# Optimization experiments

Measured on AMD Instinct MI355X. Metric: run time of the kernel, lower is better.

The kernel has to match this reference:

```python
import jax, jax.numpy as jnp
import numpy as np

EPS = 1e-9
NEG_BIG = -1e9


def setup_inputs() -> dict:
    key = jax.random.key(0)
    kq, kk, kv, km = jax.random.split(key, 4)
    B, S, D = 2, 2048, 1024
    q = jax.random.normal(kq, (B, S, D), dtype=jnp.float32)
    k = jax.random.normal(kk, (B, S, D), dtype=jnp.float32)
    v = jax.random.normal(kv, (B, S, D), dtype=jnp.float32)
    mask = jax.random.randint(km, (S, S), 0, 2, dtype=jnp.int32)
    return {"q": q, "k": k, "v": v, "mask": mask, "num_heads": 16}


def _split_heads(x, num_heads):
    B, S, D = x.shape
    # [B, S, D] -> [B, H, S, dh]
    return x.reshape(B, S, num_heads, D // num_heads).transpose(0, 2, 1, 3)


def reference(q, k, v, mask, num_heads):
    B, S, D = q.shape
    dh = D // num_heads
    scale = dh ** (-0.5)
    qh = _split_heads(q, num_heads)  # [B,H,S,dh]
    kh = _split_heads(k, num_heads)
    vh = _split_heads(v, num_heads)
    # pairwise euclidean distance (cdist, p=2): sqrt(|q|^2 + |k|^2 - 2 q.k)
    q2 = jnp.sum(qh * qh, axis=-1)  # [B,H,S]
    k2 = jnp.sum(kh * kh, axis=-1)  # [B,H,S]
    qk = jnp.einsum("bhqd,bhkd->bhqk", qh, kh)
    d2 = q2[..., :, None] + k2[..., None, :] - 2.0 * qk
    dist = jnp.sqrt(jnp.maximum(d2, 0.0)) * scale  # [B,H,S,S]
    attn = 1.0 / (dist + EPS)
    attn = attn + mask.astype(jnp.float32)[None, None] * NEG_BIG
    attn = jax.nn.softmax(attn, axis=-1)
    # dropout is identity in eval / p=0.0
    x = jnp.einsum("bhqk,bhkd->bhqd", attn, vh)
    # [B,H,S,dh] -> [B,S,D]
    return x.transpose(0, 2, 1, 3).reshape(B, S, D)
```

## Files before the change

kernel.cpp:

```cpp
#include <hip/hip_runtime.h>
#include <hip/hip_bf16.h>
#include <math.h>

namespace {

constexpr int S  = 2048;
constexpr int D  = 1024;
constexpr int H  = 16;
constexpr int DH = 64;
constexpr int QB = 32;
constexpr int KT = 64;
constexpr float NEG_BIG = -1e9f;

typedef __attribute__((ext_vector_type(8))) short short8;
typedef __attribute__((ext_vector_type(4))) float f32x4;

union Frag {
  unsigned u[4];
  short8 v;
};

__device__ __forceinline__ unsigned bf16bits(float f) {
  __hip_bfloat16 h = __float2bfloat16(f);
  unsigned short us;
  __builtin_memcpy(&us, &h, 2);
  return (unsigned)us;
}
__device__ __forceinline__ unsigned pk2(float e, float o) {
  return bf16bits(e) | (bf16bits(o) << 16);
}

#define MFMA16 __builtin_amdgcn_mfma_f32_16x16x32_bf16


__global__ __launch_bounds__(256, 2)
void euclid_attn_mfma(const float* __restrict__ qg,
                      const float* __restrict__ kg,
                      const float* __restrict__ vg,
                      const int*   __restrict__ maskg,
                      float*       __restrict__ outg) {
  const int bx = blockIdx.x;
  const int bh = blockIdx.y;
  const int b  = bh >> 4, h = bh & 15;
  const int tid  = (int)threadIdx.x;
  const int w    = tid >> 6;
  const int lane = tid & 63;
  const int x    = lane & 15;
  const int g    = lane >> 4;
  const int q0   = bx * QB;

  const float* Qb = qg + ((size_t)b * S + q0) * D + h * DH;
  const float* Kb = kg + (size_t)b * S * D + h * DH;
  const float* Vb = vg + (size_t)b * S * D + h * DH;

  const int idxk0 = (20 * g) * 4;
  const int idxe0 = (32 * (g & 1) + x) * 4;

  Frag Qhi[2][2], Qlo[2][2];
  float q2v[2];
#pragma unroll
  for (int nf = 0; nf < 2; ++nf) {
    float ss = 0.f;
#pragma unroll
    for (int s = 0; s < 2; ++s) {
      const float* p = Qb + (16 * nf + x) * D + 32 * s + 8 * g;
      float f[8];
      *(float4*)(f)     = *(const float4*)(p);
      *(float4*)(f + 4) = *(const float4*)(p + 4);
#pragma unroll
      for (int w2 = 0; w2 < 4; ++w2) {
        float e = f[2*w2], o = f[2*w2+1];
        unsigned hw = pk2(e, o);
        Qhi[nf][s].u[w2] = hw;
        float he = __uint_as_float(hw << 16);
        float ho = __uint_as_float(hw & 0xFFFF0000u);
        Qlo[nf][s].u[w2] = pk2(e - he, o - ho);
        ss += e * e + o * o;
      }
    }
    ss += __shfl_xor(ss, 16);
    ss += __shfl_xor(ss, 32);
    q2v[nf] = ss;
  }

  f32x4 acc[2][4] = {};
  float m_[2] = {-1e30f, -1e30f};
  float l_[2] = {0.f, 0.f};

  const int mrow0 = (q0 + x) * S;

  for (int t = 0; t < (S / KT) / 4; ++t) {
    const int k0 = (w + 4 * t) * KT;

    f32x4 dv[4][2];
    float rmax[2] = {-3e38f, -3e38f};

#pragma unroll
    for (int mf = 0; mf < 4; ++mf) {
      float msk[2][4];
#pragma unroll
      for (int nf = 0; nf < 2; ++nf)
#pragma unroll
        for (int r = 0; r < 4; ++r)
          msk[nf][r] =
              (float)maskg[mrow0 + 16 * nf * S + k0 + 16 * mf + 4 * g + r];

      const float* kp = Kb + (k0 + 16 * mf + x) * D + 8 * g;
      float f[16];
      *(float4*)(f)      = *(const float4*)(kp);
      *(float4*)(f + 4)  = *(const float4*)(kp + 4);
      *(float4*)(f + 8)  = *(const float4*)(kp + 32);
      *(float4*)(f + 12) = *(const float4*)(kp + 36);
      Frag khi[2], klo[2];
      float ss = 0.f;
#pragma unroll
      for (int s = 0; s < 2; ++s)
#pragma unroll
        for (int w2 = 0; w2 < 4; ++w2) {
          float e = f[8*s + 2*w2], o = f[8*s + 2*w2 + 1];
          unsigned hw = pk2(e, o);
          khi[s].u[w2] = hw;
          float he = __uint_as_float(hw << 16);
          float ho = __uint_as_float(hw & 0xFFFF0000u);
          klo[s].u[w2] = pk2(e - he, o - ho);
          ss += e * e + o * o;
        }
      ss += __shfl_xor(ss, 16);
      ss += __shfl_xor(ss, 32);
      float k2r[4];
#pragma unroll
      for (int r = 0; r < 4; ++r)
        k2r[r] = __int_as_float(
            __builtin_amdgcn_ds_bpermute(idxk0 + 4 * r, __float_as_int(ss)));

#pragma unroll
      for (int nf = 0; nf < 2; ++nf) {
        f32x4 d = {0.f, 0.f, 0.f, 0.f};
        d = MFMA16(klo[0].v, Qhi[nf][0].v, d, 0, 0, 0);
        d = MFMA16(khi[0].v, Qlo[nf][0].v, d, 0, 0, 0);
        d = MFMA16(khi[0].v, Qhi[nf][0].v, d, 0, 0, 0);
        d = MFMA16(klo[1].v, Qhi[nf][1].v, d, 0, 0, 0);
        d = MFMA16(khi[1].v, Qlo[nf][1].v, d, 0, 0, 0);
        d = MFMA16(khi[1].v, Qhi[nf][1].v, d, 0, 0, 0);
        dv[mf][nf] = d;
      }

#pragma unroll
      for (int nf = 0; nf < 2; ++nf)
#pragma unroll
        for (int r = 0; r < 4; ++r) {
          float d2 = q2v[nf] + k2r[r] - 2.f * dv[mf][nf][r];
          d2 = fmaxf(d2, 1e-8f);
          float a = 8.f * rsqrtf(d2);
          a = fmaf(msk[nf][r], NEG_BIG, a);
          dv[mf][nf][r] = a;
          rmax[nf] = fmaxf(rmax[nf], a);
        }
    }

    float corr_s[2];
#pragma unroll
    for (int nf = 0; nf < 2; ++nf) {
      float rm = rmax[nf];
      rm = fmaxf(rm, __shfl_xor(rm, 16));
      rm = fmaxf(rm, __shfl_xor(rm, 32));
      float mn   = fmaxf(m_[nf], rm);
      float corr = __expf(m_[nf] - mn);
      m_[nf] = mn;
      float rs = 0.f;
#pragma unroll
      for (int mf = 0; mf < 4; ++mf)
#pragma unroll
        for (int r = 0; r < 4; ++r) {
          float pp = __expf(dv[mf][nf][r] - mn);
          dv[mf][nf][r] = pp;
          rs += pp;
        }
      rs += __shfl_xor(rs, 16);
      rs += __shfl_xor(rs, 32);
      l_[nf] = l_[nf] * corr + rs;
      corr_s[nf] = corr;
    }

#pragma unroll
    for (int mo = 0; mo < 2; ++mo)
#pragma unroll
      for (int r = 0; r < 4; ++r) {
        float cT = __int_as_float(__builtin_amdgcn_ds_bpermute(
            idxk0 + 4 * r, __float_as_int(corr_s[mo])));
#pragma unroll
        for (int nv = 0; nv < 4; ++nv)
          acc[mo][nv][r] *= cT;
      }

    unsigned P2h[2][4][2], P2l[2][4][2];
#pragma unroll
    for (int nf = 0; nf < 2; ++nf)
#pragma unroll
      for (int mf = 0; mf < 4; ++mf)
#pragma unroll
        for (int c = 0; c < 2; ++c) {
          float p0 = dv[mf][nf][2*c], p1 = dv[mf][nf][2*c+1];
          unsigned hw = pk2(p0, p1);
          P2h[nf][mf][c] = hw;
          float he = __uint_as_float(hw << 16);
          float ho = __uint_as_float(hw & 0xFFFF0000u);
          P2l[nf][mf][c] = pk2(p0 - he, p1 - ho);
        }

    Frag afh[2][2], afl[2][2];
    const bool upper = (g >= 2);
#pragma unroll
    for (int nf = 0; nf < 2; ++nf)
#pragma unroll
      for (int s2 = 0; s2 < 2; ++s2)
#pragma unroll
        for (int w4 = 0; w4 < 4; ++w4) {
          const int c = w4 & 1;
          const int idx = idxe0 + 64 * (w4 >> 1);
          int a0 = __builtin_amdgcn_ds_bpermute(idx, (int)P2h[nf][2*s2][c]);
          int a1 = __builtin_amdgcn_ds_bpermute(idx, (int)P2h[nf][2*s2+1][c]);
          afh[nf][s2].u[w4] = (unsigned)(upper ? a1 : a0);
          int b0 = __builtin_amdgcn_ds_bpermute(idx, (int)P2l[nf][2*s2][c]);
          int b1 = __builtin_amdgcn_ds_bpermute(idx, (int)P2l[nf][2*s2+1][c]);
          afl[nf][s2].u[w4] = (unsigned)(upper ? b1 : b0);
        }

#pragma unroll
    for (int nv = 0; nv < 4; ++nv)
#pragma unroll
      for (int s2 = 0; s2 < 2; ++s2) {
        const float* vp = Vb + (k0 + 32 * s2 + 8 * g) * D + 16 * nv + x;
        float f[8];
#pragma unroll
        for (int j = 0; j < 8; ++j) f[j] = vp[j * D];
        Frag vh, vl;
#pragma unroll
        for (int w2 = 0; w2 < 4; ++w2) {
          float e = f[2*w2], o = f[2*w2+1];
          unsigned hw = pk2(e, o);
          vh.u[w2] = hw;
          float he = __uint_as_float(hw << 16);
          float ho = __uint_as_float(hw & 0xFFFF0000u);
          vl.u[w2] = pk2(e - he, o - ho);
        }
#pragma unroll
        for (int mo = 0; mo < 2; ++mo) {
          f32x4 a = acc[mo][nv];
          a = MFMA16(afl[mo][s2].v, vh.v, a, 0, 0, 0);
          a = MFMA16(afh[mo][s2].v, vl.v, a, 0, 0, 0);
          a = MFMA16(afh[mo][s2].v, vh.v, a, 0, 0, 0);
          acc[mo][nv] = a;
        }
      }
  }

  __shared__ float accs[4][QB][DH];
  __shared__ float mls[4][2][QB];
#pragma unroll
  for (int mo = 0; mo < 2; ++mo)
#pragma unroll
    for (int nv = 0; nv < 4; ++nv)
#pragma unroll
      for (int r = 0; r < 4; ++r)
        accs[w][16 * mo + 4 * g + r][16 * nv + x] = acc[mo][nv][r];
  if (g == 0) {
#pragma unroll
    for (int nf = 0; nf < 2; ++nf) {
      mls[w][0][16 * nf + x] = m_[nf];
      mls[w][1][16 * nf + x] = l_[nf];
    }
  }
  __syncthreads();

  const int qq  = tid >> 3;
  const int dh0 = (tid & 7) * 8;
  float M = -3e38f;
#pragma unroll
  for (int ww = 0; ww < 4; ++ww) M = fmaxf(M, mls[ww][0][qq]);
  float L = 0.f;
  float sw[4];
#pragma unroll
  for (int ww = 0; ww < 4; ++ww) {
    sw[ww] = __expf(mls[ww][0][qq] - M);
    L += sw[ww] * mls[ww][1][qq];
  }
  const float inv = 1.f / L;
  float o[8] = {};
#pragma unroll
  for (int ww = 0; ww < 4; ++ww)
#pragma unroll
    for (int jj = 0; jj < 8; ++jj)
      o[jj] += sw[ww] * accs[ww][qq][dh0 + jj];
#pragma unroll
  for (int jj = 0; jj < 8; ++jj) o[jj] *= inv;
  float* op = outg + ((size_t)b * S + q0 + qq) * D + h * DH + dh0;
  *(float4*)(op)     = *(float4*)(o);
  *(float4*)(op + 4) = *(float4*)(o + 4);
}

}

extern "C" void kernel_launch(void* const* d_in, const int* in_sizes, int n_in,
                              void* d_out, int out_size, void* d_ws, size_t ws_size,
                              hipStream_t stream) {
  const float* q    = (const float*)d_in[0];
  const float* k    = (const float*)d_in[1];
  const float* v    = (const float*)d_in[2];
  const int*   mask = (const int*)d_in[3];
  float* out = (float*)d_out;

  const int B = in_sizes[0] / (S * D);
  dim3 grid(S / QB, B * H);
  dim3 block(256);
  euclid_attn_mfma<<<grid, block, 0, stream>>>(q, k, v, mask, out);
}
```

Baseline: 455.6 us.

## Precompute bf16 hi/lo split K and transposed V in workspace before attention

Adds two prep kernels. One splits K into bf16 hi/lo fragments and computes |k|^2. The other transposes V and splits it into bf16 hi/lo, all stored in the workspace. A new attention kernel then loads these pre-converted fragments directly instead of converting K and V per block. This removes the conversion work that every query block repeated. It costs extra launches, extra workspace traffic, and falls back to the old kernel when the workspace is too small.

```diff
diff --git a/kernel.cpp b/kernel.cpp
--- a/kernel.cpp
+++ b/kernel.cpp
@@ -20,6 +20,26 @@
   short8 v;
 };
 
+constexpr size_t ELEMS   = (size_t)2 * H * S * DH;
+constexpr size_t OFF_KHI  = 0;
+constexpr size_t OFF_KLO  = ELEMS * 2;
+constexpr size_t OFF_VTHI = ELEMS * 4;
+constexpr size_t OFF_VTLO = ELEMS * 6;
+constexpr size_t OFF_K2   = ELEMS * 8;
+constexpr size_t WS_NEED  = ELEMS * 8 + (size_t)2 * H * S * 4;
+
+__device__ __forceinline__ unsigned fbits(float f) { return __float_as_uint(f); }
+__device__ __forceinline__ unsigned packhi(unsigned a, unsigned b) {
+  return (a >> 16) | (b & 0xFFFF0000u);
+}
+__device__ __forceinline__ void split2(float e, float o, unsigned& hi, unsigned& lo) {
+  const unsigned ue = fbits(e), uo = fbits(o);
+  hi = packhi(ue, uo);
+  const float he = __uint_as_float(ue & 0xFFFF0000u);
+  const float ho = __uint_as_float(uo & 0xFFFF0000u);
+  lo = packhi(fbits(e - he), fbits(o - ho));
+}
+
 __device__ __forceinline__ unsigned bf16bits(float f) {
   __hip_bfloat16 h = __float2bfloat16(f);
   unsigned short us;
@@ -31,6 +51,295 @@
 }
 
 #define MFMA16 __builtin_amdgcn_mfma_f32_16x16x32_bf16
+
+
+__global__ __launch_bounds__(256) void prep_k(const float* __restrict__ kin,
+                                              short8* __restrict__ khi,
+                                              short8* __restrict__ klo,
+                                              float* __restrict__ k2) {
+  const int t = blockIdx.x * 256 + (int)threadIdx.x;
+  const int c = t & 7, h = (t >> 3) & 15, s = (t >> 7) & 2047, b = t >> 18;
+  const float* p = kin + ((size_t)(b * S + s)) * D + h * DH + c * 8;
+  float f[8];
+  *(float4*)f       = *(const float4*)p;
+  *(float4*)(f + 4) = *(const float4*)(p + 4);
+  Frag hi, lo;
+  float ss = 0.f;
+#pragma unroll
+  for (int w2 = 0; w2 < 4; ++w2) {
+    split2(f[2 * w2], f[2 * w2 + 1], hi.u[w2], lo.u[w2]);
+    ss += f[2 * w2] * f[2 * w2] + f[2 * w2 + 1] * f[2 * w2 + 1];
+  }
+  const size_t o8 = ((size_t)((b * 16 + h) * S + s)) * 8 + c;
+  khi[o8] = hi.v;
+  klo[o8] = lo.v;
+  ss += __shfl_xor(ss, 1, 8);
+  ss += __shfl_xor(ss, 2, 8);
+  ss += __shfl_xor(ss, 4, 8);
+  if (c == 0) k2[(b * 16 + h) * S + s] = ss;
+}
+
+__global__ __launch_bounds__(256) void prep_vt(const float* __restrict__ vin,
+                                               short8* __restrict__ vthi,
+                                               short8* __restrict__ vtlo) {
+  __shared__ float Vs[64][65];
+  const int blk = blockIdx.x;
+  const int st = blk & 31, h = (blk >> 5) & 15, b = blk >> 9;
+  const int t = (int)threadIdx.x;
+  {
+    const int r = t >> 2, cq = t & 3;
+    const float* p = vin + ((size_t)(b * S + st * 64 + r)) * D + h * DH + cq * 16;
+#pragma unroll
+    for (int i = 0; i < 4; ++i)
+      *(float4*)&Vs[r][cq * 16 + i * 4] = *(const float4*)(p + i * 4);
+  }
+  __syncthreads();
+  const int d = t >> 2, sq = t & 3;
+  Frag h0, h1, l0, l1;
+#pragma unroll
+  for (int j = 0; j < 4; ++j)
+    split2(Vs[sq * 16 + 2 * j][d], Vs[sq * 16 + 2 * j + 1][d], h0.u[j], l0.u[j]);
+#pragma unroll
+  for (int j = 0; j < 4; ++j)
+    split2(Vs[sq * 16 + 8 + 2 * j][d], Vs[sq * 16 + 8 + 2 * j + 1][d], h1.u[j], l1.u[j]);
+  const size_t o8 = (((size_t)(b * 16 + h) * DH + d) * S + st * 64 + sq * 16) / 8;
+  vthi[o8]     = h0.v;
+  vthi[o8 + 1] = h1.v;
+  vtlo[o8]     = l0.v;
+  vtlo[o8 + 1] = l1.v;
+}
+
+
+__global__ __launch_bounds__(256, 2)
+void euclid_attn_fast(const float* __restrict__ qg,
+                      const int* __restrict__ maskg,
+                      const short8* __restrict__ khi,
+                      const short8* __restrict__ klo,
+                      const short8* __restrict__ vthi,
+                      const short8* __restrict__ vtlo,
+                      const float* __restrict__ k2g,
+                      float* __restrict__ outg) {
+  const int bx = blockIdx.x;
+  const int bh = blockIdx.y;
+  const int b  = bh >> 4;
+  const int tid  = (int)threadIdx.x;
+  const int w    = tid >> 6;
+  const int lane = tid & 63;
+  const int x    = lane & 15;
+  const int g    = lane >> 4;
+  const int q0   = bx * QB;
+
+  const float* Qb = qg + ((size_t)b * S + q0) * D + (bh & 15) * DH;
+
+  const int idxk0 = (20 * g) * 4;
+  const int idxe0 = (32 * (g & 1) + x) * 4;
+
+  Frag Qhi[2][2], Qlo[2][2];
+  float q2v[2];
+#pragma unroll
+  for (int nf = 0; nf < 2; ++nf) {
+    float ss = 0.f;
+#pragma unroll
+    for (int s = 0; s < 2; ++s) {
+      const float* p = Qb + (16 * nf + x) * D + 32 * s + 8 * g;
+      float f[8];
+      *(float4*)(f)     = *(const float4*)(p);
+      *(float4*)(f + 4) = *(const float4*)(p + 4);
+#pragma unroll
+      for (int w2 = 0; w2 < 4; ++w2) {
+        split2(f[2 * w2], f[2 * w2 + 1], Qhi[nf][s].u[w2], Qlo[nf][s].u[w2]);
+        ss += f[2 * w2] * f[2 * w2] + f[2 * w2 + 1] * f[2 * w2 + 1];
+      }
+    }
+    ss += __shfl_xor(ss, 16);
+    ss += __shfl_xor(ss, 32);
+    q2v[nf] = ss;
+  }
+
+  f32x4 acc[2][4] = {};
+  float m_[2] = {-1e30f, -1e30f};
+  float l_[2] = {0.f, 0.f};
+
+  const int mrow0 = (q0 + x) * S;
+
+  for (int t = 0; t < (S / KT) / 4; ++t) {
+    const int k0 = (w + 4 * t) * KT;
+
+    f32x4 dv[4][2];
+    float rmax[2] = {-3e38f, -3e38f};
+
+#pragma unroll
+    for (int mf = 0; mf < 4; ++mf) {
+      float mar[2][4];
+#pragma unroll
+      for (int nf = 0; nf < 2; ++nf) {
+        const int4 mi =
+            *(const int4*)(maskg + (size_t)mrow0 + 16 * nf * S + k0 + 16 * mf + 4 * g);
+        mar[nf][0] = (float)mi.x; mar[nf][1] = (float)mi.y;
+        mar[nf][2] = (float)mi.z; mar[nf][3] = (float)mi.w;
+      }
+
+      const size_t kb8 = ((size_t)bh * S + k0 + 16 * mf + x) * 8;
+      Frag kh[2], kl[2];
+      kh[0].v = khi[kb8 + g];
+      kh[1].v = khi[kb8 + 4 + g];
+      kl[0].v = klo[kb8 + g];
+      kl[1].v = klo[kb8 + 4 + g];
+
+      const float4 k2r = *(const float4*)(k2g + (size_t)bh * S + k0 + 16 * mf + 4 * g);
+      const float k2a[4] = {k2r.x, k2r.y, k2r.z, k2r.w};
+
+#pragma unroll
+      for (int nf = 0; nf < 2; ++nf) {
+        f32x4 d = {0.f, 0.f, 0.f, 0.f};
+        d = MFMA16(kl[0].v, Qhi[nf][0].v, d, 0, 0, 0);
+        d = MFMA16(kh[0].v, Qlo[nf][0].v, d, 0, 0, 0);
+        d = MFMA16(kh[0].v, Qhi[nf][0].v, d, 0, 0, 0);
+        d = MFMA16(kl[1].v, Qhi[nf][1].v, d, 0, 0, 0);
+        d = MFMA16(kh[1].v, Qlo[nf][1].v, d, 0, 0, 0);
+        d = MFMA16(kh[1].v, Qhi[nf][1].v, d, 0, 0, 0);
+        dv[mf][nf] = d;
+      }
+
+#pragma unroll
+      for (int nf = 0; nf < 2; ++nf)
+#pragma unroll
+        for (int r = 0; r < 4; ++r) {
+          float d2 = q2v[nf] + k2a[r] - 2.f * dv[mf][nf][r];
+          d2 = fmaxf(d2, 1e-8f);
+          float a = 8.f * rsqrtf(d2);
+          a = fmaf(mar[nf][r], NEG_BIG, a);
+          dv[mf][nf][r] = a;
+          rmax[nf] = fmaxf(rmax[nf], a);
+        }
+    }
+
+    float corr_s[2];
+#pragma unroll
+    for (int nf = 0; nf < 2; ++nf) {
+      float rm = rmax[nf];
+      rm = fmaxf(rm, __shfl_xor(rm, 16));
+      rm = fmaxf(rm, __shfl_xor(rm, 32));
+      float mn   = fmaxf(m_[nf], rm);
+      float corr = __expf(m_[nf] - mn);
+      m_[nf] = mn;
+      float rs = 0.f;
+#pragma unroll
+      for (int mf = 0; mf < 4; ++mf)
+#pragma unroll
+        for (int r = 0; r < 4; ++r) {
+          float pp = __expf(dv[mf][nf][r] - mn);
+          dv[mf][nf][r] = pp;
+          rs += pp;
+        }
+      rs += __shfl_xor(rs, 16);
+      rs += __shfl_xor(rs, 32);
+      l_[nf] = l_[nf] * corr + rs;
+      corr_s[nf] = corr;
+    }
+
+#pragma unroll
+    for (int mo = 0; mo < 2; ++mo)
+#pragma unroll
+      for (int r = 0; r < 4; ++r) {
+        float cT = __int_as_float(__builtin_amdgcn_ds_bpermute(
+            idxk0 + 4 * r, __float_as_int(corr_s[mo])));
+#pragma unroll
+        for (int nv = 0; nv < 4; ++nv)
+          acc[mo][nv][r] *= cT;
+      }
+
+    unsigned P2h[2][4][2], P2l[2][4][2];
+#pragma unroll
+    for (int nf = 0; nf < 2; ++nf)
+#pragma unroll
+      for (int mf = 0; mf < 4; ++mf)
+#pragma unroll
+        for (int c = 0; c < 2; ++c)
+          split2(dv[mf][nf][2 * c], dv[mf][nf][2 * c + 1],
+                 P2h[nf][mf][c], P2l[nf][mf][c]);
+
+    Frag afh[2][2], afl[2][2];
+    const bool upper = (g >= 2);
+#pragma unroll
+    for (int nf = 0; nf < 2; ++nf)
+#pragma unroll
+      for (int s2 = 0; s2 < 2; ++s2)
+#pragma unroll
+        for (int w4 = 0; w4 < 4; ++w4) {
+          const int c = w4 & 1;
+          const int idx = idxe0 + 64 * (w4 >> 1);
+          int a0 = __builtin_amdgcn_ds_bpermute(idx, (int)P2h[nf][2 * s2][c]);
+          int a1 = __builtin_amdgcn_ds_bpermute(idx, (int)P2h[nf][2 * s2 + 1][c]);
+          afh[nf][s2].u[w4] = (unsigned)(upper ? a1 : a0);
+          int b0 = __builtin_amdgcn_ds_bpermute(idx, (int)P2l[nf][2 * s2][c]);
+          int b1 = __builtin_amdgcn_ds_bpermute(idx, (int)P2l[nf][2 * s2 + 1][c]);
+          afl[nf][s2].u[w4] = (unsigned)(upper ? b1 : b0);
+        }
+
+#pragma unroll
+    for (int nv = 0; nv < 4; ++nv)
+#pragma unroll
+      for (int s2 = 0; s2 < 2; ++s2) {
+        const size_t vt8 =
+            (((size_t)bh * DH + 16 * nv + x) * S + k0 + 32 * s2 + 8 * g) / 8;
+        Frag vh, vl;
+        vh.v = vthi[vt8];
+        vl.v = vtlo[vt8];
+#pragma unroll
+        for (int mo = 0; mo < 2; ++mo) {
+          f32x4 a = acc[mo][nv];
+          a = MFMA16(afl[mo][s2].v, vh.v, a, 0, 0, 0);
+          a = MFMA16(afh[mo][s2].v, vl.v, a, 0, 0, 0);
+          a = MFMA16(afh[mo][s2].v, vh.v, a, 0, 0, 0);
+          acc[mo][nv] = a;
+        }
+      }
+  }
+
+  __shared__ float accs[4][QB][DH];
+  __shared__ float mls[4][2][QB];
+#pragma unroll
+  for (int mo = 0; mo < 2; ++mo)
+#pragma unroll
+    for (int nv = 0; nv < 4; ++nv)
+#pragma unroll
+      for (int r = 0; r < 4; ++r)
+        accs[w][16 * mo + 4 * g + r][16 * nv + x] = acc[mo][nv][r];
+  if (g == 0) {
+#pragma unroll
+    for (int nf = 0; nf < 2; ++nf) {
+      mls[w][0][16 * nf + x] = m_[nf];
+      mls[w][1][16 * nf + x] = l_[nf];
+    }
+  }
+  __syncthreads();
+
+  const int qq  = tid >> 3;
+  const int dh0 = (tid & 7) * 8;
+  float M = -3e38f;
+#pragma unroll
+  for (int ww = 0; ww < 4; ++ww) M = fmaxf(M, mls[ww][0][qq]);
+  float L = 0.f;
+  float sw[4];
+#pragma unroll
+  for (int ww = 0; ww < 4; ++ww) {
+    sw[ww] = __expf(mls[ww][0][qq] - M);
+    L += sw[ww] * mls[ww][1][qq];
+  }
+  const float inv = 1.f / L;
+  float o[8] = {};
+#pragma unroll
+  for (int ww = 0; ww < 4; ++ww)
+#pragma unroll
+    for (int jj = 0; jj < 8; ++jj)
+      o[jj] += sw[ww] * accs[ww][qq][dh0 + jj];
+#pragma unroll
+  for (int jj = 0; jj < 8; ++jj) o[jj] *= inv;
+  float* op = outg + ((size_t)b * S + q0 + qq) * D + (bh & 15) * DH + dh0;
+  *(float4*)(op)     = *(float4*)(o);
+  *(float4*)(op + 4) = *(float4*)(o + 4);
+}
 
 
 __global__ __launch_bounds__(256, 2)
@@ -313,5 +622,19 @@
   const int B = in_sizes[0] / (S * D);
   dim3 grid(S / QB, B * H);
   dim3 block(256);
-  euclid_attn_mfma<<<grid, block, 0, stream>>>(q, k, v, mask, out);
-}
+
+  if (B == 2 && d_ws != nullptr && ws_size >= WS_NEED) {
+    char* ws = (char*)d_ws;
+    short8* khi  = (short8*)(ws + OFF_KHI);
+    short8* klo  = (short8*)(ws + OFF_KLO);
+    short8* vthi = (short8*)(ws + OFF_VTHI);
+    short8* vtlo = (short8*)(ws + OFF_VTLO);
+    float*  k2   = (float*)(ws + OFF_K2);
+    prep_k<<<2048, 256, 0, stream>>>(k, khi, klo, k2);
+    prep_vt<<<1024, 256, 0, stream>>>(v, vthi, vtlo);
+    euclid_attn_fast<<<grid, block, 0, stream>>>(q, mask, khi, klo, vthi, vtlo,
+                                                 k2, out);
+  } else {
+    euclid_attn_mfma<<<grid, block, 0, stream>>>(q, k, v, mask, out);
+  }
+}
```

Result: faster. 413.5 us (-9.2%).
